# Kernel optimization log

Measured on AMD Instinct MI355X. Metric: run time of the kernel, lower is better.

## Reference

```python
import jax, jax.numpy as jnp
import numpy as np
from jax import lax

N = 2048
NUM_CLASSES = 21  # background + 20 classes


def xy_to_cxcy(xy):
    return jnp.concatenate([(xy[:, 2:] + xy[:, :2]) / 2.0, xy[:, 2:] - xy[:, :2]], axis=-1)


def cxcy_to_xy(c):
    return jnp.concatenate([c[:, :2] - c[:, 2:] / 2.0, c[:, :2] + c[:, 2:] / 2.0], axis=-1)


def gcxgcy_to_cxcy(g, priors_cxcy):
    # offsets already pre-scaled (/10, /20) by the caller, matching the torch forward
    return jnp.concatenate([g[:, :2] * priors_cxcy[:, 2:] + priors_cxcy[:, :2],
                            jnp.exp(g[:, 2:]) * priors_cxcy[:, 2:]], axis=-1)


def pairwise_iou(a, b):
    # a: [N,4], b: [M,4] corner format -> [N,M]
    lt = jnp.maximum(a[:, None, :2], b[None, :, :2])
    rb = jnp.minimum(a[:, None, 2:], b[None, :, 2:])
    wh = jnp.clip(rb - lt, 0.0)
    inter = wh[..., 0] * wh[..., 1]
    area_a = (a[:, 2] - a[:, 0]) * (a[:, 3] - a[:, 1])
    area_b = (b[:, 2] - b[:, 0]) * (b[:, 3] - b[:, 1])
    return inter / (area_a[:, None] + area_b[None, :] - inter)


def _detect(rois_xy, predicted_locs, predicted_scores, min_score, max_overlap, top_k):
    n = rois_xy.shape[0]
    rois_cxcy = xy_to_cxcy(rois_xy)
    locs = predicted_locs.reshape(n, -1, 4)                      # [N, C, 4]
    probs = jax.nn.softmax(predicted_scores, axis=1)             # [N, C]
    best = jnp.argmax(probs, axis=1)                             # locs for argmax class
    g = jnp.take_along_axis(locs, best[:, None, None], axis=1)[:, 0, :]
    g = jnp.concatenate([g[:, :2] / 10.0, g[:, 2:] / 20.0], axis=-1)
    decoded = cxcy_to_xy(gcxgcy_to_cxcy(g, rois_cxcy))           # [N, 4]

    def nms_class(cls_scores):
        valid = cls_scores > min_score
        s = jnp.where(valid, cls_scores, -jnp.inf)
        order = jnp.argsort(-s)                                  # desc; invalid last
        s_sorted = s[order]
        b_sorted = decoded[order]
        ov = lax.stop_gradient(pairwise_iou(b_sorted, b_sorted))  # [N, N]
        sup0 = ~valid[order]                                     # invalid start suppressed

        def body(i, sup):
            new = jnp.logical_or(sup, ov[i] > max_overlap)
            new = new.at[i].set(False)                           # never self-suppress
            return jnp.where(sup[i], sup, new)                   # skip already-suppressed

        sup = lax.fori_loop(0, n, body, sup0)
        return b_sorted, jnp.where(~sup, s_sorted, -jnp.inf)

    # vmap the greedy NMS over the 20 foreground classes
    boxes_c, scores_c = jax.vmap(nms_class)(probs[:, 1:].T)      # [20,N,4], [20,N]
    labels_c = jnp.broadcast_to(jnp.arange(1, NUM_CLASSES)[:, None], scores_c.shape)

    fs = scores_c.reshape(-1)
    fb = boxes_c.reshape(-1, 4)
    fl = labels_c.reshape(-1)
    topv, topi = lax.top_k(fs, top_k)
    ok = jnp.isfinite(topv)
    out_boxes = jnp.where(ok[:, None], fb[topi],
                          jnp.array([0.0, 0.0, 1.0, 1.0], dtype=fb.dtype))
    out_labels = jnp.where(ok, fl[topi], 0)
    out_scores = jnp.where(ok, topv, 0.0)
    return out_boxes, out_labels, out_scores


def setup_inputs() -> dict:
    key = jax.random.key(0)
    k1, k2, k3, k4 = jax.random.split(key, 4)
    cxcy = jax.random.uniform(k1, (N, 2), minval=0.1, maxval=0.9)
    wh = jax.random.uniform(k2, (N, 2), minval=0.05, maxval=0.3)
    rois_xy = jnp.concatenate([cxcy - wh / 2.0, cxcy + wh / 2.0], axis=-1)
    predicted_locs = jax.random.normal(k3, (N, NUM_CLASSES * 4), dtype=jnp.float32) * 0.5
    predicted_scores = jax.random.normal(k4, (N, NUM_CLASSES), dtype=jnp.float32) * 2.0
    return {"rois_xy": rois_xy,
            "predicted_locs": predicted_locs,
            "predicted_scores": predicted_scores,
            "min_score": jnp.float32(0.01),
            "max_overlap": jnp.float32(0.45),
            "top_k": 100}


def reference(rois_xy, predicted_locs, predicted_scores, min_score, max_overlap, top_k):
    return _detect(rois_xy, predicted_locs, predicted_scores, min_score, max_overlap, top_k)
```

## Files before the change

### kernel.cpp

```cpp
#include <hip/hip_runtime.h>
#include <cstdint>

#define NROI 2048
#define NCLS 21
#define NFG  20
#define CPAD 128
#define CTOT (NFG * CPAD)
#define NTHR 512
#define SBLK 256
#define RSEL 480
#define SCAP 512
#define CSEL 512
#define DROWS 64
#define INVH 0xFF800000u

typedef unsigned long long u64;
typedef unsigned int u32;

__device__ __forceinline__ u32 desc_key(float s) {
  u32 u = __float_as_uint(s);
  u32 asc = (u & 0x80000000u) ? ~u : (u | 0x80000000u);
  return ~asc;
}
__device__ __forceinline__ float key_to_float(u32 desc) {
  u32 asc = ~desc;
  u32 u = (asc & 0x80000000u) ? (asc ^ 0x80000000u) : ~asc;
  return __uint_as_float(u);
}
__device__ __forceinline__ u64 shflx_u64(u64 v, int m) {
  u32 lo = (u32)v, hi = (u32)(v >> 32);
  lo = (u32)__shfl_xor((int)lo, m);
  hi = (u32)__shfl_xor((int)hi, m);
  return ((u64)hi << 32) | (u64)lo;
}
__device__ __forceinline__ void cmpex64(u64& mine, u64 other, int i, int j, int k) {
  bool amIlow = ((i & j) == 0);
  bool dir = ((i & k) == 0);
  bool otherLess = other < mine;
  if (otherLess != (amIlow != dir)) mine = other;
}

__device__ __forceinline__ void bucket_select(const int* h, int need, int lane,
                                              int* outB, int* outC) {
  int base = lane << 2;
  int c0 = h[base], c1 = h[base + 1], c2 = h[base + 2], c3 = h[base + 3];
  int s = c0 + c1 + c2 + c3;
  int pre = s;
  #pragma unroll
  for (int off = 1; off < 64; off <<= 1) {
    int v = __shfl_up(pre, off);
    if (lane >= off) pre += v;
  }
  u64 ball = __ballot(pre >= need);
  int ln = __ffsll((long long)ball) - 1;
  int exc = __shfl(pre, ln) - __shfl(s, ln);
  int b0 = __shfl(c0, ln), b1 = __shfl(c1, ln), b2 = __shfl(c2, ln);
  int bkt, cb;
  if (exc + b0 >= need)                { bkt = (ln << 2) + 0; cb = exc; }
  else if (exc + b0 + b1 >= need)      { bkt = (ln << 2) + 1; cb = exc + b0; }
  else if (exc + b0 + b1 + b2 >= need) { bkt = (ln << 2) + 2; cb = exc + b0 + b1; }
  else                                 { bkt = (ln << 2) + 3; cb = exc + b0 + b1 + b2; }
  if (lane == 0) { *outB = bkt; *outC = cb; }
}

__global__ __launch_bounds__(64)
void k_decode(const float* __restrict__ rois,
              const float* __restrict__ locs,
              const float* __restrict__ scores,
              float* __restrict__ probsT,
              float4* __restrict__ decoded,
              u32* __restrict__ done) {
  __shared__ float srow[DROWS][NCLS + 2];
  const int tid = threadIdx.x;
  const int rbase = blockIdx.x * DROWS;
  if (rbase == 0 && tid == 0) *done = 0u;

  const float* src = scores + (size_t)rbase * NCLS;
  for (int t = tid; t < DROWS * NCLS; t += 64)
    srow[t / NCLS][t % NCLS] = src[t];
  __syncthreads();

  const int r = rbase + tid;
  float s[NCLS];
  #pragma unroll
  for (int c = 0; c < NCLS; ++c) s[c] = srow[tid][c];
  float m = s[0];
  #pragma unroll
  for (int c = 0; c < NCLS; ++c) m = fmaxf(m, s[c]);
  float sum = 0.0f;
  #pragma unroll
  for (int c = 0; c < NCLS; ++c) { s[c] = expf(s[c] - m); sum += s[c]; }

  float pb = s[0] / sum; int best = 0;
  #pragma unroll
  for (int c = 1; c < NCLS; ++c) {
    float p = s[c] / sum;
    probsT[(c - 1) * NROI + r] = p;
    if (p > pb) { pb = p; best = c; }
  }

  float4 roi = ((const float4*)rois)[r];
  float pcx = __fmul_rn(__fadd_rn(roi.x, roi.z), 0.5f);
  float pcy = __fmul_rn(__fadd_rn(roi.y, roi.w), 0.5f);
  float pw  = __fsub_rn(roi.z, roi.x);
  float ph  = __fsub_rn(roi.w, roi.y);

  float4 gl = ((const float4*)locs)[r * NCLS + best];
  float g0 = gl.x / 10.0f;
  float g1 = gl.y / 10.0f;
  float g2 = gl.z / 20.0f;
  float g3 = gl.w / 20.0f;

  float cx = __fadd_rn(__fmul_rn(g0, pw), pcx);
  float cy = __fadd_rn(__fmul_rn(g1, ph), pcy);
  float w  = __fmul_rn(expf(g2), pw);
  float h  = __fmul_rn(expf(g3), ph);
  float hw = __fmul_rn(w, 0.5f);
  float hh = __fmul_rn(h, 0.5f);
  decoded[r] = make_float4(__fsub_rn(cx, hw), __fsub_rn(cy, hh),
                           __fadd_rn(cx, hw), __fadd_rn(cy, hh));
}

__global__ __launch_bounds__(NTHR)
void k_nms(const float* __restrict__ probsT,
           const float4* __restrict__ decoded,
           const float* __restrict__ min_score_p,
           const float* __restrict__ max_overlap_p,
           u64* __restrict__ cand,
           float4* __restrict__ cbox,
           u32* __restrict__ done,
           float* __restrict__ out,
           const int* __restrict__ top_k_p) {
  __shared__ u32 LDSW[7296];
  __shared__ u64 remInitW[4];
  __shared__ int hist1[256], hist2[256];
  __shared__ int cntLds, scLds, cSelSh, selB1, selC1, selB2, selD2, mSh, cCnt;
  __shared__ u32 lastSh;

  u64* mbAu    = (u64*)(LDSW + 0);
  u64* mbBu    = (u64*)(LDSW + 1024);
  u64* skeyW64 = (u64*)(LDSW + 2048);
  u64* maskW   = (u64*)(LDSW + 3072);
  float* bx0   = (float*)(LDSW + 5120);
  float* by0   = (float*)(LDSW + 5376);
  float* bx1   = (float*)(LDSW + 5632);
  float* by1   = (float*)(LDSW + 5888);
  float* areaA = (float*)(LDSW + 6144);
  float* sx0   = (float*)(LDSW + 6400);
  float* sy0   = (float*)(LDSW + 6528);
  float* sx1   = (float*)(LDSW + 6656);
  float* sy1   = (float*)(LDSW + 6784);
  float* sarea = (float*)(LDSW + 6912);
  u32* survKeyH = LDSW + 7040;
  u32* survRows = LDSW + 7168;

  const int cls = blockIdx.x;
  const int tid = threadIdx.x;
  const int lane = tid & 63;
  const int wid = tid >> 6;
  const float msc = *min_score_p;
  const float ovr = *max_overlap_p;
  const int K = *top_k_p;
  const int Kcap = (K < CPAD) ? K : CPAD;

  if (tid == 0) { cntLds = 0; scLds = 0; }
  __syncthreads();

  float pA = probsT[cls * NROI + tid];
  float pB = probsT[cls * NROI + tid + 512];
  float pC = probsT[cls * NROI + tid + 1024];
  float pD = probsT[cls * NROI + tid + 1536];
  bool vA = pA > msc, vB = pB > msc, vC = pC > msc, vD = pD > msc;
  u64 kqA = ((u64)desc_key(vA ? pA : -__builtin_inff()) << 32) | (u32)tid;
  u64 kqB = ((u64)desc_key(vB ? pB : -__builtin_inff()) << 32) | (u32)(tid + 512);
  u64 kqC = ((u64)desc_key(vC ? pC : -__builtin_inff()) << 32) | (u32)(tid + 1024);
  u64 kqD = ((u64)desc_key(vD ? pD : -__builtin_inff()) << 32) | (u32)(tid + 1536);
  {
    u64 ba = __ballot(vA), bb = __ballot(vB);
    u64 bc = __ballot(vC), bd = __ballot(vD);
    if (lane == 0)
      atomicAdd(&cntLds, __popcll(ba) + __popcll(bb) + __popcll(bc) + __popcll(bd));
  }
  __syncthreads();
  const int nv = cntLds;

  int sc = 0;
  int processed = 0;
  u64 minKey = 0ULL;

  while (sc < Kcap && processed < nv) {
    int rem = nv - processed;
    int need = (rem < RSEL) ? rem : RSEL;

    if (tid < 256) { hist1[tid] = 0; hist2[tid] = 0; }
    if (tid == 0) cSelSh = 0;
    __syncthreads();
    bool valA = (kqA > minKey) && ((u32)(kqA >> 32) < INVH);
    bool valB = (kqB > minKey) && ((u32)(kqB >> 32) < INVH);
    bool valC = (kqC > minKey) && ((u32)(kqC >> 32) < INVH);
    bool valD = (kqD > minKey) && ((u32)(kqD >> 32) < INVH);
    if (valA) atomicAdd(&hist1[(int)((kqA >> 56) & 255)], 1);
    if (valB) atomicAdd(&hist1[(int)((kqB >> 56) & 255)], 1);
    if (valC) atomicAdd(&hist1[(int)((kqC >> 56) & 255)], 1);
    if (valD) atomicAdd(&hist1[(int)((kqD >> 56) & 255)], 1);
    __syncthreads();
    if (wid == 0) bucket_select(hist1, need, lane, &selB1, &selC1);
    __syncthreads();
    const int B1 = selB1, C1 = selC1;
    if (valA && (int)((kqA >> 56) & 255) == B1)
      atomicAdd(&hist2[(int)((kqA >> 48) & 255)], 1);
    if (valB && (int)((kqB >> 56) & 255) == B1)
      atomicAdd(&hist2[(int)((kqB >> 48) & 255)], 1);
    if (valC && (int)((kqC >> 56) & 255) == B1)
      atomicAdd(&hist2[(int)((kqC >> 48) & 255)], 1);
    if (valD && (int)((kqD >> 56) & 255) == B1)
      atomicAdd(&hist2[(int)((kqD >> 48) & 255)], 1);
    __syncthreads();
    if (wid == 0) bucket_select(hist2, need - C1, lane, &selB2, &selD2);
    __syncthreads();
    const int pred16 = (selB1 << 8) | selB2;

    bool sA = valA && (int)((kqA >> 48) & 0xFFFF) <= pred16;
    bool sB = valB && (int)((kqB >> 48) & 0xFFFF) <= pred16;
    bool sC = valC && (int)((kqC >> 48) & 0xFFFF) <= pred16;
    bool sD = valD && (int)((kqD >> 48) & 0xFFFF) <= pred16;
    {
      u64 bA = __ballot(sA), bB = __ballot(sB);
      u64 bC = __ballot(sC), bD = __ballot(sD);
      int cnt = __popcll(bA) + __popcll(bB) + __popcll(bC) + __popcll(bD);
      int basePos = 0;
      if (lane == 0) basePos = cnt ? atomicAdd(&cSelSh, cnt) : 0;
      basePos = __shfl(basePos, 0);
      u64 lm = (1ULL << lane) - 1ULL;
      int pA_ = basePos + __popcll(bA & lm);
      int pB_ = basePos + __popcll(bA) + __popcll(bB & lm);
      int pC_ = basePos + __popcll(bA) + __popcll(bB) + __popcll(bC & lm);
      int pD_ = basePos + __popcll(bA) + __popcll(bB) + __popcll(bC) + __popcll(bD & lm);
      if (sA && pA_ < SCAP) mbAu[pA_] = kqA;
      if (sB && pB_ < SCAP) mbAu[pB_] = kqB;
      if (sC && pC_ < SCAP) mbAu[pC_] = kqC;
      if (sD && pD_ < SCAP) mbAu[pD_] = kqD;
    }
    __syncthreads();
    int Csel = cSelSh; if (Csel > SCAP) Csel = SCAP;
    if (tid >= Csel) mbAu[tid] = ~0ULL;
    __syncthreads();

    u64 key = mbAu[tid];
    int parity = 0;
    auto ldsp = [&](int k, int j) {
      u64* buf = parity ? mbBu : mbAu; parity ^= 1;
      buf[tid] = key;
      __syncthreads();
      u64 o = buf[tid ^ j];
      cmpex64(key, o, tid, j, k);
    };
    auto shfp = [&](int k, int j) {
      u64 o = shflx_u64(key, j);
      cmpex64(key, o, tid, j, k);
    };
    for (int k = 2; k <= 64; k <<= 1)
      for (int j = k >> 1; j >= 1; j >>= 1) shfp(k, j);
    ldsp(128, 64);
    for (int j = 32; j >= 1; j >>= 1) shfp(128, j);
    ldsp(256, 128); ldsp(256, 64);
    for (int j = 32; j >= 1; j >>= 1) shfp(256, j);
    ldsp(512, 256); ldsp(512, 128); ldsp(512, 64);
    for (int j = 32; j >= 1; j >>= 1) shfp(512, j);
    skeyW64[tid] = key;
    __syncthreads();

    for (int base = 0; base < Csel && sc < Kcap; base += SBLK) {
      int RL = Csel - base; if (RL > SBLK) RL = SBLK;
      if (tid < SBLK) {
        int p = base + tid; if (p > Csel - 1) p = Csel - 1;
        u64 kq = skeyW64[p];
        float4 b = decoded[(u32)kq];
        bx0[tid] = b.x; by0[tid] = b.y; bx1[tid] = b.z; by1[tid] = b.w;
        areaA[tid] = __fmul_rn(__fsub_rn(b.z, b.x), __fsub_rn(b.w, b.y));
      }
      if (tid < 4) remInitW[tid] = 0ULL;
      __syncthreads();

      if (sc > 0 && tid < SBLK) {
        float jx0 = bx0[tid], jy0 = by0[tid], jx1 = bx1[tid], jy1 = by1[tid];
        float ab = areaA[tid];
        bool kill = false;
        for (int u = 0; u < sc; ++u) {
          float ix0 = sx0[u], iy0 = sy0[u], ix1 = sx1[u], iy1 = sy1[u];
          float ia = sarea[u];
          float lx = fmaxf(ix0, jx0), ly = fmaxf(iy0, jy0);
          float rx = fminf(ix1, jx1), ry = fminf(iy1, jy1);
          float w_ = fmaxf(__fsub_rn(rx, lx), 0.0f);
          float h_ = fmaxf(__fsub_rn(ry, ly), 0.0f);
          float inter = __fmul_rn(w_, h_);
          float iou = __fdiv_rn(inter, __fsub_rn(__fadd_rn(ia, ab), inter));
          kill = kill || (iou > ovr);
        }
        u64 bal = __ballot(kill);
        if (lane == 0) remInitW[wid] = bal;
      }
      __syncthreads();

      {
        int nw = (RL + 63) >> 6;
        for (int r2 = wid; r2 < RL; r2 += 8) {
          if ((remInitW[r2 >> 6] >> (r2 & 63)) & 1ULL) continue;
          float ix0 = bx0[r2], iy0 = by0[r2], ix1 = bx1[r2], iy1 = by1[r2];
          float ia = areaA[r2];
          for (int ct = (r2 >> 6); ct < nw; ++ct) {
            int j = (ct << 6) + lane;
            float jx0 = bx0[j], jy0 = by0[j], jx1 = bx1[j], jy1 = by1[j];
            float ab = areaA[j];
            float lx = fmaxf(ix0, jx0), ly = fmaxf(iy0, jy0);
            float rx = fminf(ix1, jx1), ry = fminf(iy1, jy1);
            float w_ = fmaxf(__fsub_rn(rx, lx), 0.0f);
            float h_ = fmaxf(__fsub_rn(ry, ly), 0.0f);
            float inter = __fmul_rn(w_, h_);
            float iou = __fdiv_rn(inter, __fsub_rn(__fadd_rn(ia, ab), inter));
            bool bit = iou > ovr;
            if (ct == (r2 >> 6)) bit = bit && (j > r2);
            u64 bal = __ballot(bit);
            if (lane == 0) maskW[(r2 << 2) + ct] = bal;
          }
        }
      }
      __syncthreads();

      if (wid == 0) {
        int t0 = RL;
        u64 rw0 = (t0 <= 0) ? ~0ULL : ((t0 >= 64) ? 0ULL : (~0ULL << t0));
        int t1 = t0 - 64;
        u64 rw1 = (t1 <= 0) ? ~0ULL : ((t1 >= 64) ? 0ULL : (~0ULL << t1));
        int t2 = t0 - 128;
        u64 rw2 = (t2 <= 0) ? ~0ULL : ((t2 >= 64) ? 0ULL : (~0ULL << t2));
        int t3 = t0 - 192;
        u64 rw3 = (t3 <= 0) ? ~0ULL : ((t3 >= 64) ? 0ULL : (~0ULL << t3));
        rw0 |= remInitW[0]; rw1 |= remInitW[1];
        rw2 |= remInitW[2]; rw3 |= remInitW[3];
        int scW = sc;
        bool full = scW >= Kcap;
        u64 a00,a01,a02,a03,a10,a11,a12,a13,a20,a21,a22,a23,a30,a31,a32,a33;
        u64 b00,b01,b02,b03,b10,b11,b12,b13,b20,b21,b22,b23,b30,b31,b32,b33;
#define LD4(V0,V1,V2,V3,R) { int rr_ = (R); \
        V0 = maskW[(rr_<<2)+0]; V1 = maskW[(rr_<<2)+1]; \
        V2 = maskW[(rr_<<2)+2]; V3 = maskW[(rr_<<2)+3]; }
#define PRX(RWG, BIT, M0,M1,M2,M3, ROW) \
        if (!full && !(((RWG) >> (BIT)) & 1ULL)) { \
          rw0 |= (M0); rw1 |= (M1); rw2 |= (M2); rw3 |= (M3); \
          if (lane == 0) survRows[scW] = (u32)(base + (ROW)); \
          ++scW; full = (scW >= Kcap); \
        }
#define SWEEPG(G, RWG) \
        if (!full && (((G) << 6) < RL)) { \
          const int rb = (G) << 6; \
          LD4(a00,a01,a02,a03, rb+0) LD4(a10,a11,a12,a13, rb+1) \
          LD4(a20,a21,a22,a23, rb+2) LD4(a30,a31,a32,a33, rb+3) \
          for (int bb = 0; bb < 64 && !full; bb += 4) { \
            LD4(b00,b01,b02,b03, rb+bb+4) LD4(b10,b11,b12,b13, rb+bb+5) \
            LD4(b20,b21,b22,b23, rb+bb+6) LD4(b30,b31,b32,b33, rb+bb+7) \
            PRX(RWG, bb+0, a00,a01,a02,a03, rb+bb+0) \
            PRX(RWG, bb+1, a10,a11,a12,a13, rb+bb+1) \
            PRX(RWG, bb+2, a20,a21,a22,a23, rb+bb+2) \
            PRX(RWG, bb+3, a30,a31,a32,a33, rb+bb+3) \
            a00=b00;a01=b01;a02=b02;a03=b03; a10=b10;a11=b11;a12=b12;a13=b13; \
            a20=b20;a21=b21;a22=b22;a23=b23; a30=b30;a31=b31;a32=b32;a33=b33; \
          } \
        }
        SWEEPG(0, rw0) SWEEPG(1, rw1) SWEEPG(2, rw2) SWEEPG(3, rw3)
#undef SWEEPG
#undef PRX
#undef LD4
        if (lane == 0) scLds = scW;
      }
      __syncthreads();

      {
        int scNew = scLds;
        if (tid >= sc && tid < scNew) {
          int wrow = (int)survRows[tid];
          int rr = wrow - base;
          sx0[tid] = bx0[rr]; sy0[tid] = by0[rr];
          sx1[tid] = bx1[rr]; sy1[tid] = by1[rr];
          sarea[tid] = areaA[rr];
          survKeyH[tid] = (u32)(skeyW64[wrow] >> 32);
        }
        __syncthreads();
        sc = scNew;
      }
    }

    minKey = skeyW64[Csel - 1];
    processed += Csel;
    __syncthreads();
  }

  if (tid < CPAD) {
    int o = cls * CPAD + tid;
    if (tid < sc) {
      cand[o] = ((u64)survKeyH[tid] << 32) | (u32)o;
      cbox[o] = make_float4(sx0[tid], sy0[tid], sx1[tid], sy1[tid]);
    } else {
      cand[o] = ~0ULL;
    }
  }

  __threadfence();
  __syncthreads();
  if (tid == 0) lastSh = atomicAdd(done, 1u);
  __syncthreads();
  if (lastSh != NFG - 1) return;
  __threadfence();

  u64* kk = (u64*)LDSW;
  u64* ck = (u64*)(LDSW + 5120);
  if (tid == 0) cCnt = 0;
  if (tid < 256) { hist1[tid] = 0; hist2[tid] = 0; }
  __syncthreads();
  for (int t = tid; t < CTOT; t += NTHR) {
    u64 v = cand[t];
    kk[t] = v;
    if (v != ~0ULL) atomicAdd(&hist1[(int)(v >> 56)], 1);
  }
  __syncthreads();
  if (wid == 0) {
    int b4 = lane << 2;
    int s = hist1[b4] + hist1[b4 + 1] + hist1[b4 + 2] + hist1[b4 + 3];
    #pragma unroll
    for (int off = 32; off; off >>= 1) s += __shfl_xor(s, off);
    if (lane == 0) mSh = s;
  }
  __syncthreads();
  const int M = mSh;
  const int Kneed = (K < M) ? K : M;

  if (Kneed > 0) {
    if (wid == 0) bucket_select(hist1, Kneed, lane, &selB1, &selC1);
    __syncthreads();
    const int B1 = selB1, C1 = selC1;
    for (int t = tid; t < CTOT; t += NTHR) {
      u64 v = kk[t];
      if (v != ~0ULL && (int)(v >> 56) == B1)
        atomicAdd(&hist2[(int)((v >> 48) & 255)], 1);
    }
    __syncthreads();
    if (wid == 0) bucket_select(hist2, Kneed - C1, lane, &selB2, &selD2);
    __syncthreads();
    const int B2 = selB2;
    for (int t = tid; t < CTOT; t += NTHR) {
      u64 v = kk[t];
      if (v == ~0ULL) continue;
      int b1 = (int)(v >> 56);
      int b2 = (int)((v >> 48) & 255);
      if (b1 < B1 || (b1 == B1 && b2 <= B2)) {
        int pos = atomicAdd(&cCnt, 1);
        if (pos < CSEL) ck[pos] = v;
      }
    }
    __syncthreads();
    const int C = cCnt;
    if (C <= CSEL) {
      if (tid < C) {
        u64 my = ck[tid];
        int rank = 0;
        for (int u = 0; u < C; ++u) rank += (ck[u] < my) ? 1 : 0;
        if (rank < K) {
          u32 flat = (u32)(my & 0xFFFFFFFFu);
          float score = key_to_float((u32)(my >> 32));
          int c2 = (int)(flat >> 7);
          float4 b = cbox[flat];
          out[rank * 4 + 0] = b.x;
          out[rank * 4 + 1] = b.y;
          out[rank * 4 + 2] = b.z;
          out[rank * 4 + 3] = b.w;
          out[K * 4 + rank] = (float)(c2 + 1);
          out[K * 5 + rank] = score;
        }
      }
    } else {
      for (int t = tid; t < CTOT; t += NTHR) {
        u64 kap = kk[t];
        if (kap == ~0ULL) continue;
        int rank = 0;
        #pragma unroll
        for (int cc2 = 0; cc2 < NFG; ++cc2) {
          const u64* a = kk + cc2 * CPAD;
          int lb = 0;
          #pragma unroll
          for (int s2 = CPAD >> 1; s2; s2 >>= 1) {
            int pq = lb + s2;
            if (a[pq - 1] < kap) lb = pq;
          }
          rank += lb;
        }
        if (rank < K) {
          u32 flat = (u32)(kap & 0xFFFFFFFFu);
          float score = key_to_float((u32)(kap >> 32));
          int c2 = (int)(flat >> 7);
          float4 b = cbox[flat];
          out[rank * 4 + 0] = b.x;
          out[rank * 4 + 1] = b.y;
          out[rank * 4 + 2] = b.z;
          out[rank * 4 + 3] = b.w;
          out[K * 4 + rank] = (float)(c2 + 1);
          out[K * 5 + rank] = score;
        }
      }
    }
  }
  __syncthreads();
  for (int r = tid; r < K; r += NTHR) {
    if (r >= M) {
      out[r * 4 + 0] = 0.0f; out[r * 4 + 1] = 0.0f;
      out[r * 4 + 2] = 1.0f; out[r * 4 + 3] = 1.0f;
      out[K * 4 + r] = 0.0f;
      out[K * 5 + r] = 0.0f;
    }
  }
}

extern "C" void kernel_launch(void* const* d_in, const int* in_sizes, int n_in,
                              void* d_out, int out_size, void* d_ws, size_t ws_size,
                              hipStream_t stream) {
  const float* rois        = (const float*)d_in[0];
  const float* locs        = (const float*)d_in[1];
  const float* scores      = (const float*)d_in[2];
  const float* min_score   = (const float*)d_in[3];
  const float* max_overlap = (const float*)d_in[4];
  const int*   top_k       = (const int*)d_in[5];

  char* ws = (char*)d_ws;
  u64*    cand    = (u64*)ws;
  float4* cbox    = (float4*)(ws + 20480);
  float*  probsT  = (float*)(ws + 20480 + 40960);
  float4* decoded = (float4*)(ws + 20480 + 40960 + 163840);
  u32*    done    = (u32*)(ws + 20480 + 40960 + 163840 + 32768);

  k_decode<<<NROI / DROWS, 64, 0, stream>>>(rois, locs, scores, probsT, decoded, done);
  k_nms<<<NFG, NTHR, 0, stream>>>(probsT, decoded, min_score, max_overlap,
                                  cand, cbox, done, (float*)d_out, top_k);
}
```

Baseline: 57.22 us.

## Fuse decode and NMS kernels into one launch with spin-wait counter

Merges the softmax/decode kernel into the NMS kernel. The first four blocks of 512 threads each decode 512 ROIs and then bump a global counter. The remaining 20 class blocks spin on that counter with an acquire load before reading the probabilities. The goal is to save a kernel launch and the inter-kernel gap. In exchange it adds a memset, a larger LDS allocation, and a reliance on all blocks being co-resident, which holds for 24 blocks. Decode also runs on far fewer, larger blocks, which reduces its parallelism.

```diff
diff --git a/kernel.cpp b/kernel.cpp
--- a/kernel.cpp
+++ b/kernel.cpp
@@ -4,6 +4,7 @@
 #define NROI 2048
 #define NCLS 21
 #define NFG  20
+#define NDEC 4
 #define CPAD 128
 #define CTOT (NFG * CPAD)
 #define NTHR 512
@@ -11,7 +12,6 @@
 #define RSEL 480
 #define SCAP 512
 #define CSEL 512
-#define DROWS 64
 #define INVH 0xFF800000u
 
 typedef unsigned long long u64;
@@ -63,79 +63,81 @@
   if (lane == 0) { *outB = bkt; *outC = cb; }
 }
 
-__global__ __launch_bounds__(64)
-void k_decode(const float* __restrict__ rois,
-              const float* __restrict__ locs,
-              const float* __restrict__ scores,
-              float* __restrict__ probsT,
-              float4* __restrict__ decoded,
-              u32* __restrict__ done) {
-  __shared__ float srow[DROWS][NCLS + 2];
-  const int tid = threadIdx.x;
-  const int rbase = blockIdx.x * DROWS;
-  if (rbase == 0 && tid == 0) *done = 0u;
-
-  const float* src = scores + (size_t)rbase * NCLS;
-  for (int t = tid; t < DROWS * NCLS; t += 64)
-    srow[t / NCLS][t % NCLS] = src[t];
-  __syncthreads();
-
-  const int r = rbase + tid;
-  float s[NCLS];
-  #pragma unroll
-  for (int c = 0; c < NCLS; ++c) s[c] = srow[tid][c];
-  float m = s[0];
-  #pragma unroll
-  for (int c = 0; c < NCLS; ++c) m = fmaxf(m, s[c]);
-  float sum = 0.0f;
-  #pragma unroll
-  for (int c = 0; c < NCLS; ++c) { s[c] = expf(s[c] - m); sum += s[c]; }
-
-  float pb = s[0] / sum; int best = 0;
-  #pragma unroll
-  for (int c = 1; c < NCLS; ++c) {
-    float p = s[c] / sum;
-    probsT[(c - 1) * NROI + r] = p;
-    if (p > pb) { pb = p; best = c; }
-  }
-
-  float4 roi = ((const float4*)rois)[r];
-  float pcx = __fmul_rn(__fadd_rn(roi.x, roi.z), 0.5f);
-  float pcy = __fmul_rn(__fadd_rn(roi.y, roi.w), 0.5f);
-  float pw  = __fsub_rn(roi.z, roi.x);
-  float ph  = __fsub_rn(roi.w, roi.y);
-
-  float4 gl = ((const float4*)locs)[r * NCLS + best];
-  float g0 = gl.x / 10.0f;
-  float g1 = gl.y / 10.0f;
-  float g2 = gl.z / 20.0f;
-  float g3 = gl.w / 20.0f;
-
-  float cx = __fadd_rn(__fmul_rn(g0, pw), pcx);
-  float cy = __fadd_rn(__fmul_rn(g1, ph), pcy);
-  float w  = __fmul_rn(expf(g2), pw);
-  float h  = __fmul_rn(expf(g3), ph);
-  float hw = __fmul_rn(w, 0.5f);
-  float hh = __fmul_rn(h, 0.5f);
-  decoded[r] = make_float4(__fsub_rn(cx, hw), __fsub_rn(cy, hh),
-                           __fadd_rn(cx, hw), __fadd_rn(cy, hh));
-}
-
 __global__ __launch_bounds__(NTHR)
-void k_nms(const float* __restrict__ probsT,
-           const float4* __restrict__ decoded,
+void k_all(const float* __restrict__ rois,
+           const float* __restrict__ locs,
+           const float* __restrict__ scores,
            const float* __restrict__ min_score_p,
            const float* __restrict__ max_overlap_p,
+           float* __restrict__ probsT,
+           float4* __restrict__ decoded,
            u64* __restrict__ cand,
            float4* __restrict__ cbox,
-           u32* __restrict__ done,
+           u32* __restrict__ ctr,
            float* __restrict__ out,
            const int* __restrict__ top_k_p) {
-  __shared__ u32 LDSW[7296];
+  __shared__ u32 LDSW[11776];
   __shared__ u64 remInitW[4];
   __shared__ int hist1[256], hist2[256];
   __shared__ int cntLds, scLds, cSelSh, selB1, selC1, selB2, selD2, mSh, cCnt;
   __shared__ u32 lastSh;
+
+  const int tid = threadIdx.x;
+  const int lane = tid & 63;
+  const int wid = tid >> 6;
+
+  if (blockIdx.x < NDEC) {
+    float* stg = (float*)LDSW;
+    const int rbase = blockIdx.x * 512;
+    const float* src = scores + (size_t)rbase * NCLS;
+    for (int t = tid; t < 512 * NCLS; t += NTHR)
+      stg[(t / NCLS) * 23 + (t % NCLS)] = src[t];
+    __syncthreads();
+
+    const int r = rbase + tid;
+    float s[NCLS];
+    #pragma unroll
+    for (int c = 0; c < NCLS; ++c) s[c] = stg[tid * 23 + c];
+    float m = s[0];
+    #pragma unroll
+    for (int c = 0; c < NCLS; ++c) m = fmaxf(m, s[c]);
+    float sum = 0.0f;
+    #pragma unroll
+    for (int c = 0; c < NCLS; ++c) { s[c] = expf(s[c] - m); sum += s[c]; }
+
+    float pb = s[0] / sum; int best = 0;
+    #pragma unroll
+    for (int c = 1; c < NCLS; ++c) {
+      float p = s[c] / sum;
+      probsT[(c - 1) * NROI + r] = p;
+      if (p > pb) { pb = p; best = c; }
+    }
+
+    float4 roi = ((const float4*)rois)[r];
+    float pcx = __fmul_rn(__fadd_rn(roi.x, roi.z), 0.5f);
+    float pcy = __fmul_rn(__fadd_rn(roi.y, roi.w), 0.5f);
+    float pw  = __fsub_rn(roi.z, roi.x);
+    float ph  = __fsub_rn(roi.w, roi.y);
+
+    float4 gl = ((const float4*)locs)[r * NCLS + best];
+    float g0 = gl.x / 10.0f;
+    float g1 = gl.y / 10.0f;
+    float g2 = gl.z / 20.0f;
+    float g3 = gl.w / 20.0f;
+
+    float cx = __fadd_rn(__fmul_rn(g0, pw), pcx);
+    float cy = __fadd_rn(__fmul_rn(g1, ph), pcy);
+    float w  = __fmul_rn(expf(g2), pw);
+    float h  = __fmul_rn(expf(g3), ph);
+    float hw = __fmul_rn(w, 0.5f);
+    float hh = __fmul_rn(h, 0.5f);
+    decoded[r] = make_float4(__fsub_rn(cx, hw), __fsub_rn(cy, hh),
+                             __fadd_rn(cx, hw), __fadd_rn(cy, hh));
+    __threadfence();
+    __syncthreads();
+    if (tid == 0) atomicAdd(&ctr[1], 1u);
+    return;
+  }
 
   u64* mbAu    = (u64*)(LDSW + 0);
   u64* mbBu    = (u64*)(LDSW + 1024);
@@ -154,17 +156,23 @@
   u32* survKeyH = LDSW + 7040;
   u32* survRows = LDSW + 7168;
 
-  const int cls = blockIdx.x;
-  const int tid = threadIdx.x;
-  const int lane = tid & 63;
-  const int wid = tid >> 6;
+  const int cls = blockIdx.x - NDEC;
   const float msc = *min_score_p;
   const float ovr = *max_overlap_p;
   const int K = *top_k_p;
   const int Kcap = (K < CPAD) ? K : CPAD;
 
   if (tid == 0) { cntLds = 0; scLds = 0; }
-  __syncthreads();
+
+  if (tid == 0) {
+    u32 v;
+    do {
+      __builtin_amdgcn_s_sleep(2);
+      v = __hip_atomic_load(&ctr[1], __ATOMIC_ACQUIRE, __HIP_MEMORY_SCOPE_AGENT);
+    } while (v < (u32)NDEC);
+  }
+  __syncthreads();
+  __threadfence();
 
   float pA = probsT[cls * NROI + tid];
   float pB = probsT[cls * NROI + tid + 512];
@@ -407,7 +415,7 @@
 
   __threadfence();
   __syncthreads();
-  if (tid == 0) lastSh = atomicAdd(done, 1u);
+  if (tid == 0) lastSh = atomicAdd(&ctr[0], 1u);
   __syncthreads();
   if (lastSh != NFG - 1) return;
   __threadfence();
@@ -534,9 +542,10 @@
   float4* cbox    = (float4*)(ws + 20480);
   float*  probsT  = (float*)(ws + 20480 + 40960);
   float4* decoded = (float4*)(ws + 20480 + 40960 + 163840);
-  u32*    done    = (u32*)(ws + 20480 + 40960 + 163840 + 32768);
-
-  k_decode<<<NROI / DROWS, 64, 0, stream>>>(rois, locs, scores, probsT, decoded, done);
-  k_nms<<<NFG, NTHR, 0, stream>>>(probsT, decoded, min_score, max_overlap,
-                                  cand, cbox, done, (float*)d_out, top_k);
-}
+  u32*    ctr     = (u32*)(ws + 20480 + 40960 + 163840 + 32768);
+
+  hipMemsetAsync(ctr, 0, 8, stream);
+  k_all<<<NDEC + NFG, NTHR, 0, stream>>>(rois, locs, scores, min_score,
+                                         max_overlap, probsT, decoded,
+                                         cand, cbox, ctr, (float*)d_out, top_k);
+}
```

Measured after the change: 69.39 us. 21.3% more time.
